# Kernel tuning notes

Hardware: AMD Instinct MI355X
Metric: run time of the kernel (lower is better)

The kernel has to match this reference:

```python
import jax, jax.numpy as jnp
import numpy as np

_J6 = jnp.array([[0, 0, 0, 0, 0, 1], [0, 0, 0, 0, -1, 0], [0, 0, 0, 1, 0, 0],
                 [0, 0, 1, 0, 0, 0], [0, -1, 0, 0, 0, 0], [1, 0, 0, 0, 0, 0]], dtype=jnp.float32)
_PAIRS4 = [(0, 1), (0, 2), (0, 3), (1, 2), (1, 3), (2, 3)]


def exterior(p1, p2):
    # p1, p2: (B,T,H,4) -> (B,T,H,6) normalized Pluecker line coordinates
    parts = [p1[..., i] * p2[..., j] - p1[..., j] * p2[..., i] for i, j in _PAIRS4]
    L = jnp.stack(parts, axis=-1)
    n = jnp.sqrt(jnp.sum(L * L, axis=-1, keepdims=True))
    return L / jnp.maximum(n, 1e-12)


def setup_inputs() -> dict:
    D, H = 1024, 16
    B, T = 2, 2048
    key = jax.random.key(0)
    ks = jax.random.split(key, 16)
    s = 0.02
    return {
        'x': jax.random.normal(ks[0], (B, T, D), dtype=jnp.float32),
        'qkv_w': jax.random.normal(ks[1], (D, 3 * D), dtype=jnp.float32) * s,
        'qkv_b': jnp.zeros((3 * D,), dtype=jnp.float32),
        'w1_write': jax.random.normal(ks[2], (D, 4 * H), dtype=jnp.float32) * s,
        'w2_write': jax.random.normal(ks[3], (D, 4 * H), dtype=jnp.float32) * s,
        'w1_read': jax.random.normal(ks[4], (D, 4 * H), dtype=jnp.float32) * s,
        'w2_read': jax.random.normal(ks[5], (D, 4 * H), dtype=jnp.float32) * s,
        'geo_w': jax.random.normal(ks[6], (D, D), dtype=jnp.float32) * s,
        'geo_b': jnp.zeros((D,), dtype=jnp.float32),
        'gate_w': jax.random.normal(ks[7], (D, H), dtype=jnp.float32) * s,
        'gate_b': jnp.zeros((H,), dtype=jnp.float32),
        'inc_scale': jnp.ones((H,), dtype=jnp.float32),
        'out_w': jax.random.normal(ks[8], (D, D), dtype=jnp.float32) * s,
        'out_b': jnp.zeros((D,), dtype=jnp.float32),
    }


def reference(x, qkv_w, qkv_b, w1_write, w2_write, w1_read, w2_read,
              geo_w, geo_b, gate_w, gate_b, inc_scale, out_w, out_b):
    B, T, D = x.shape
    H = inc_scale.shape[0]
    dh = D // H
    scale = dh ** -0.5

    qkv = (x @ qkv_w + qkv_b).reshape(B, T, 3, H, dh)
    qkv = jnp.transpose(qkv, (2, 0, 3, 1, 4))  # (3,B,H,T,dh)
    q, k, v = qkv[0], qkv[1], qkv[2]

    std_logits = jnp.einsum('bhqd,bhkd->bhqk', q, k) * scale

    x_prev = jnp.concatenate([jnp.zeros((B, 1, D), dtype=x.dtype), x[:, :-1]], axis=1)
    w1 = (x_prev @ w1_write).reshape(B, T, H, 4)
    w2 = (x @ w2_write).reshape(B, T, H, 4)
    write_lines = exterior(w1, w2)  # (B,T,H,6)
    r1 = (x @ w1_read).reshape(B, T, H, 4)
    r2 = (x @ w2_read).reshape(B, T, H, 4)
    read_lines = exterior(r1, r2)  # (B,T,H,6)

    J_write = jnp.einsum('bthi,ij->bthj', write_lines, _J6)  # (B,T,H,6)
    geo_logits = jnp.einsum('bqhi,bkhi->bhqk', read_lines, J_write)
    geo_logits = geo_logits * inc_scale.reshape(1, H, 1, 1)

    mask = jnp.triu(jnp.ones((T, T), dtype=bool), k=1)  # True above diagonal
    neg = jnp.float32(-jnp.inf)

    std_attn = jax.nn.softmax(jnp.where(mask, neg, std_logits), axis=-1)
    std_out = jnp.einsum('bhqk,bhkd->bqhd', std_attn, v).reshape(B, T, D)

    geo_attn = jax.nn.softmax(jnp.where(mask, neg, geo_logits), axis=-1)
    geo_v = (x @ geo_w + geo_b).reshape(B, T, H, dh)
    geo_out = jnp.einsum('bhqk,bkhd->bqhd', geo_attn, geo_v).reshape(B, T, D)

    gate = jax.nn.sigmoid(x @ gate_w + gate_b)  # (B,T,H)
    gate = jnp.mean(gate, axis=-1, keepdims=True)  # (B,T,1)

    combined = (1.0 - gate) * std_out + gate * geo_out
    return combined @ out_w + out_b
```

## Files before the change

### kernel.cpp

```cpp
#include <hip/hip_runtime.h>
#include <hip/hip_bf16.h>

#define Bc 2
#define Tc 2048
#define Dc 1024
#define Hc 16
#define Mc (Bc*Tc)
#define QB 64
#define KB 32
#define NALL 4480

typedef __attribute__((ext_vector_type(8))) short bf16x8;
typedef __attribute__((ext_vector_type(4))) short bf16x4;
typedef __attribute__((ext_vector_type(4))) float fx4;

__device__ __forceinline__ short f2bf(float f) {
  __hip_bfloat16 h = __float2bfloat16(f);
  return *reinterpret_cast<short*>(&h);
}
__device__ __forceinline__ float bf2f(short s) {
  unsigned int u = ((unsigned int)(unsigned short)s) << 16;
  float f;
  __builtin_memcpy(&f, &u, 4);
  return f;
}
__device__ __forceinline__ short p2bf(float f) {
  unsigned int u;
  __builtin_memcpy(&u, &f, 4);
  return (short)((u + 0x8000u) >> 16);
}
__device__ __forceinline__ int pk2bf(float a, float b) {
  unsigned int ua, ub;
  __builtin_memcpy(&ua, &a, 4);
  __builtin_memcpy(&ub, &b, 4);
  return (int)(((ua + 0x8000u) >> 16) | (((ub + 0x8000u) >> 16) << 16));
}

#define MFMA(a, b, c) __builtin_amdgcn_mfma_f32_16x16x32_bf16((a), (b), (c), 0, 0, 0)

#define GLD16(G, L) __builtin_amdgcn_global_load_lds( \
    (const __attribute__((address_space(1))) unsigned int*)(G), \
    (__attribute__((address_space(3))) unsigned int*)(L), 16, 0, 0)

__global__ __launch_bounds__(256) void prep_k(
    const float* __restrict__ x,
    const float* __restrict__ qkv_w, const float* __restrict__ geow,
    const float* __restrict__ w1w, const float* __restrict__ w2w,
    const float* __restrict__ w1r, const float* __restrict__ w2r,
    const float* __restrict__ gatew, const float* __restrict__ outw,
    const float* __restrict__ qkv_b, const float* __restrict__ geob,
    const float* __restrict__ gateb,
    short* __restrict__ xb, short* __restrict__ wtall,
    short* __restrict__ wtout, float* __restrict__ ball)
{
  __shared__ float tile[32][33];
  const int blk = blockIdx.x;

  if (blk < 4096) {
    const int i = blk * 256 + threadIdx.x;
    const float4 v = ((const float4*)x)[i];
    bf16x4 o;
    o[0] = f2bf(v.x); o[1] = f2bf(v.y); o[2] = f2bf(v.z); o[3] = f2bf(v.w);
    ((bf16x4*)xb)[i] = o;
    return;
  }
  if (blk < 8576) {
    const int b2 = blk - 4096;
    const int n0 = (b2 % 140) * 32, k0 = (b2 / 140) * 32;
    const int tx = threadIdx.x & 31, ty = threadIdx.x >> 5;
    const int n = n0 + tx;
    const float* src = nullptr; int ln = 0, sN = 0;
    if (n < 3072)      { src = qkv_w; ln = n;        sN = 3072; }
    else if (n < 4096) { src = geow;  ln = n - 3072; sN = 1024; }
    else if (n < 4160) { src = w1w;   ln = n - 4096; sN = 64; }
    else if (n < 4224) { src = w2w;   ln = n - 4160; sN = 64; }
    else if (n < 4288) { src = w1r;   ln = n - 4224; sN = 64; }
    else if (n < 4352) { src = w2r;   ln = n - 4288; sN = 64; }
    else if (n < 4368) { src = gatew; ln = n - 4352; sN = 16; }
    #pragma unroll
    for (int i = 0; i < 4; i++)
      tile[ty * 4 + i][tx] = src ? src[(size_t)(k0 + ty * 4 + i) * sN + ln] : 0.f;
    __syncthreads();
    #pragma unroll
    for (int i = 0; i < 4; i++) {
      const int nn = n0 + ty * 4 + i;
      const float s = (nn < 1024) ? 0.125f : 1.f;
      wtall[(size_t)nn * 1024 + k0 + tx] = f2bf(tile[tx][ty * 4 + i] * s);
    }
    return;
  }
  if (blk < 9600) {
    const int b3 = blk - 8576;
    const int n0 = (b3 & 31) * 32, k0 = (b3 >> 5) * 32;
    const int tx = threadIdx.x & 31, ty = threadIdx.x >> 5;
    #pragma unroll
    for (int i = 0; i < 4; i++)
      tile[ty * 4 + i][tx] = outw[(size_t)(k0 + ty * 4 + i) * 1024 + n0 + tx];
    __syncthreads();
    #pragma unroll
    for (int i = 0; i < 4; i++)
      wtout[(size_t)(n0 + ty * 4 + i) * 1024 + k0 + tx] = f2bf(tile[tx][ty * 4 + i]);
    return;
  }
  {
    const int n = (blk - 9600) * 256 + threadIdx.x;
    if (n >= NALL) return;
    float v = 0.f;
    if (n < 1024)      v = qkv_b[n] * 0.125f;
    else if (n < 3072) v = qkv_b[n];
    else if (n < 4096) v = geob[n - 3072];
    else if (n >= 4352 && n < 4368) v = gateb[n - 4352];
    ball[n] = v;
  }
}

template<bool BF16_OUT>
__global__ __launch_bounds__(256) void gemm_mfma_k(
    const short* __restrict__ A, const short* __restrict__ Bt,
    const float* __restrict__ bias, void* __restrict__ Cv,
    int M, int N, int K)
{
  __shared__ short As[128][32];
  __shared__ short Bs[128][32];
  const int orig = blockIdx.x + blockIdx.y * gridDim.x;
  const int q8 = (gridDim.x * gridDim.y) >> 3;
  const int idx = (orig & 7) * q8 + (orig >> 3);
  const int m0 = (idx / gridDim.x) * 128, n0 = (idx % gridDim.x) * 128;
  const int tid = threadIdx.x;
  const int wave = tid >> 6, lane = tid & 63;
  const int l15 = lane & 15, lg = lane >> 4;
  const int wm = wave >> 1, wn = wave & 1;
  const int srow = lane >> 2;
  const int schk = (lane & 3) * 8;

  const size_t aBase = (size_t)(m0 + wave * 16 + srow) * K + schk;
  const size_t bBase = (size_t)(n0 + wave * 16 + srow) * K + schk;

  fx4 acc[4][4] = {};

  for (int k0 = 0; k0 < K; k0 += 32) {
    __syncthreads();
    GLD16(&A[aBase + k0],              &As[wave * 16][0]);
    GLD16(&A[aBase + (size_t)64 * K + k0], &As[64 + wave * 16][0]);
    GLD16(&Bt[bBase + k0],             &Bs[wave * 16][0]);
    GLD16(&Bt[bBase + (size_t)64 * K + k0], &Bs[64 + wave * 16][0]);
    __syncthreads();
    bf16x8 af[4], bf[4];
    #pragma unroll
    for (int i = 0; i < 4; i++) {
      af[i] = *(const bf16x8*)&As[wm * 64 + i * 16 + l15][8 * lg];
      bf[i] = *(const bf16x8*)&Bs[wn * 64 + i * 16 + l15][8 * lg];
    }
    #pragma unroll
    for (int i = 0; i < 4; i++)
      #pragma unroll
      for (int j = 0; j < 4; j++)
        acc[i][j] = MFMA(af[i], bf[j], acc[i][j]);
  }

  #pragma unroll
  for (int i = 0; i < 4; i++)
    #pragma unroll
    for (int j = 0; j < 4; j++) {
      const int n = n0 + wn * 64 + j * 16 + l15;
      const float bv = bias ? bias[n] : 0.f;
      #pragma unroll
      for (int rg = 0; rg < 4; rg++) {
        const int m = m0 + wm * 64 + i * 16 + lg * 4 + rg;
        const float v = acc[i][j][rg] + bv;
        if constexpr (BF16_OUT)
          ((short*)Cv)[(size_t)m * N + n] = f2bf(v);
        else
          ((float*)Cv)[(size_t)m * N + n] = v;
      }
    }
}

template<bool BF16_OUT>
__global__ __launch_bounds__(256) void gemm_mfma64_k(
    const short* __restrict__ A, const short* __restrict__ Bt,
    const float* __restrict__ bias, void* __restrict__ Cv,
    int M, int N, int K)
{
  __shared__ short As[64][32];
  __shared__ short Bs[128][32];
  const int orig = blockIdx.x + blockIdx.y * gridDim.x;
  const int q8 = (gridDim.x * gridDim.y) >> 3;
  const int idx = (orig & 7) * q8 + (orig >> 3);
  const int m0 = (idx / gridDim.x) * 64, n0 = (idx % gridDim.x) * 128;
  const int tid = threadIdx.x;
  const int wave = tid >> 6, lane = tid & 63;
  const int l15 = lane & 15, lg = lane >> 4;
  const int srow = lane >> 2;
  const int schk = (lane & 3) * 8;

  const size_t aBase = (size_t)(m0 + wave * 16 + srow) * K + schk;
  const size_t bBase = (size_t)(n0 + wave * 16 + srow) * K + schk;

  fx4 acc[4][2] = {};

  for (int k0 = 0; k0 < K; k0 += 32) {
    __syncthreads();
    GLD16(&A[aBase + k0],                   &As[wave * 16][0]);
    GLD16(&Bt[bBase + k0],                  &Bs[wave * 16][0]);
    GLD16(&Bt[bBase + (size_t)64 * K + k0], &Bs[64 + wave * 16][0]);
    __syncthreads();
    bf16x8 af[4], bf[2];
    #pragma unroll
    for (int i = 0; i < 4; i++)
      af[i] = *(const bf16x8*)&As[i * 16 + l15][8 * lg];
    #pragma unroll
    for (int j = 0; j < 2; j++)
      bf[j] = *(const bf16x8*)&Bs[wave * 32 + j * 16 + l15][8 * lg];
    #pragma unroll
    for (int i = 0; i < 4; i++)
      #pragma unroll
      for (int j = 0; j < 2; j++)
        acc[i][j] = MFMA(af[i], bf[j], acc[i][j]);
  }

  #pragma unroll
  for (int i = 0; i < 4; i++)
    #pragma unroll
    for (int j = 0; j < 2; j++) {
      const int n = n0 + wave * 32 + j * 16 + l15;
      const float bv = bias ? bias[n] : 0.f;
      #pragma unroll
      for (int rg = 0; rg < 4; rg++) {
        const int m = m0 + i * 16 + lg * 4 + rg;
        const float v = acc[i][j][rg] + bv;
        if constexpr (BF16_OUT)
          ((short*)Cv)[(size_t)m * N + n] = f2bf(v);
        else
          ((float*)Cv)[(size_t)m * N + n] = v;
      }
    }
}

__device__ __forceinline__ void exterior6(const float a[4], const float c[4], float L[6]) {
  L[0] = a[0]*c[1] - a[1]*c[0];
  L[1] = a[0]*c[2] - a[2]*c[0];
  L[2] = a[0]*c[3] - a[3]*c[0];
  L[3] = a[1]*c[2] - a[2]*c[1];
  L[4] = a[1]*c[3] - a[3]*c[1];
  L[5] = a[2]*c[3] - a[3]*c[2];
}

__device__ __forceinline__ void load4bf(const short* p, float o[4]) {
  const bf16x4 v = *(const bf16x4*)p;
  o[0] = bf2f(v[0]); o[1] = bf2f(v[1]); o[2] = bf2f(v[2]); o[3] = bf2f(v[3]);
}

__global__ void lines_k(const short* __restrict__ allb,
                        const float* __restrict__ incs,
                        short* __restrict__ JWb, short* __restrict__ RLb,
                        float* __restrict__ gatev)
{
  const int idx = blockIdx.x * 256 + threadIdx.x;
  if (idx >= Bc * Tc * Hc) return;
  const int h = idx & 15;
  const int t = (idx >> 4) & (Tc - 1);
  const int b = idx >> 15;
  const size_t row = (size_t)b * Tc + t;
  const size_t lrow = ((size_t)(b * Hc + h) * Tc + t) * 8;

  float a[4] = {0.f, 0.f, 0.f, 0.f};
  float c[4];
  load4bf(&allb[row * NALL + 4160 + h * 4], c);
  if (t > 0) load4bf(&allb[(row - 1) * NALL + 4096 + h * 4], a);

  float L[6];
  exterior6(a, c, L);
  float n = sqrtf(L[0]*L[0] + L[1]*L[1] + L[2]*L[2] + L[3]*L[3] + L[4]*L[4] + L[5]*L[5]);
  float inv = 1.f / fmaxf(n, 1e-12f);
  const float s = incs[h];
  bf16x8 jw;
  jw[0] = f2bf( L[5] * inv * s);
  jw[1] = f2bf(-L[4] * inv * s);
  jw[2] = f2bf( L[3] * inv * s);
  jw[3] = f2bf( L[2] * inv * s);
  jw[4] = f2bf(-L[1] * inv * s);
  jw[5] = f2bf( L[0] * inv * s);
  jw[6] = 0; jw[7] = 0;
  *(bf16x8*)&JWb[lrow] = jw;

  load4bf(&allb[row * NALL + 4224 + h * 4], a);
  load4bf(&allb[row * NALL + 4288 + h * 4], c);
  exterior6(a, c, L);
  n = sqrtf(L[0]*L[0] + L[1]*L[1] + L[2]*L[2] + L[3]*L[3] + L[4]*L[4] + L[5]*L[5]);
  inv = 1.f / fmaxf(n, 1e-12f);
  bf16x8 rl;
  #pragma unroll
  for (int i = 0; i < 6; i++) rl[i] = f2bf(L[i] * inv);
  rl[6] = 0; rl[7] = 0;
  *(bf16x8*)&RLb[lrow] = rl;

  if (h == 0) {
    float ssum = 0.f;
    #pragma unroll
    for (int hh = 0; hh < 16; hh++) {
      const float v = bf2f(allb[row * NALL + 4352 + hh]);
      ssum += 1.f / (1.f + __expf(-v));
    }
    gatev[row] = ssum * (1.f / 16.f);
  }
}

#define LOADK(K0, a0, a1, b0, b1) { \
  const size_t rb0 = (size_t)(b * Tc + (K0) + l15) * NALL + 1024 + h * 64; \
  const size_t rb1 = rb0 + (size_t)16 * NALL; \
  a0 = *(const bf16x8*)&allb[rb0 + lg * 8]; \
  a1 = *(const bf16x8*)&allb[rb0 + 32 + lg * 8]; \
  b0 = *(const bf16x8*)&allb[rb1 + lg * 8]; \
  b1 = *(const bf16x8*)&allb[rb1 + 32 + lg * 8]; }

#define LOADJW(K0, j0, j1) { \
  j0 = z8; j1 = z8; \
  if (lg == 0) { \
    j0 = *(const bf16x8*)&JWb[(size_t)(bh * Tc + (K0) + l15) * 8]; \
    j1 = *(const bf16x8*)&JWb[(size_t)(bh * Tc + (K0) + 16 + l15) * 8]; \
  } }

#define LOADVG(K0, vr, gr) { \
  vr = *(const bf16x8*)&allb[(size_t)(b * Tc + (K0) + kk) * NALL + 2048 + h * 64 + dg]; \
  gr = *(const bf16x8*)&allb[(size_t)(b * Tc + (K0) + kk) * NALL + 3072 + h * 64 + dg]; }

#define STAGEVG(CUR, vr, gr) { \
  _Pragma("unroll") for (int j = 0; j < 8; j++) { \
    const int d = dg + j; \
    Vt[CUR][d][pcol] = vr[j]; Gt[CUR][d][pcol] = gr[j]; \
  } }

#define COMPUTE(K0, CUR, ka0, ka1, kb0, kb1, jw0, jw1) \
  if ((K0) <= qhi) { \
    fx4 z = {0.f, 0.f, 0.f, 0.f}; \
    fx4 sS0, sS1, sG0, sG1; \
    __builtin_amdgcn_s_setprio(1); \
    sS0 = MFMA(qf0, ka0, z); sS0 = MFMA(qf1, ka1, sS0); \
    sS1 = MFMA(qf0, kb0, z); sS1 = MFMA(qf1, kb1, sS1); \
    sG0 = MFMA(rlf, jw0, z); sG1 = MFMA(rlf, jw1, z); \
    __builtin_amdgcn_s_setprio(0); \
    if ((K0) + KB - 1 > q0 + wave * 16) { \
      const int kg0 = (K0) + l15, kg1 = (K0) + 16 + l15; \
      _Pragma("unroll") for (int r = 0; r < 4; r++) { \
        const int qg = q0 + wave * 16 + lg * 4 + r; \
        if (kg0 > qg) { sS0[r] = -1e30f; sG0[r] = -1e30f; } \
        if (kg1 > qg) { sS1[r] = -1e30f; sG1[r] = -1e30f; } \
      } } \
    _Pragma("unroll") for (int r = 0; r < 4; r++) { \
      const int ql = lg * 4 + r; \
      const float p0 = __expf(sS0[r]); const float p1 = __expf(sS1[r]); \
      lpS[r] += p0 + p1; \
      *(int*)&Ps[wave][ql][2 * l15] = pk2bf(p0, p1); \
      const float g0 = __expf(sG0[r]); const float g1 = __expf(sG1[r]); \
      lpG[r] += g0 + g1; \
      *(int*)&Pg[wave][ql][2 * l15] = pk2bf(g0, g1); \
    } \
    const bf16x8 pa  = *(const bf16x8*)&Ps[wave][l15][8 * lg]; \
    const bf16x8 pga = *(const bf16x8*)&Pg[wave][l15][8 * lg]; \
    __builtin_amdgcn_s_setprio(1); \
    _Pragma("unroll") for (int dt = 0; dt < 4; dt++) { \
      const int dV = dt * 16 + l15; \
      const int swz = 8 * (lg ^ ((dV >> 3) & 3)); \
      accS[dt] = MFMA(pa,  *(const bf16x8*)&Vt[CUR][dV][swz], accS[dt]); \
      accG[dt] = MFMA(pga, *(const bf16x8*)&Gt[CUR][dV][swz], accG[dt]); \
    } \
    __builtin_amdgcn_s_setprio(0); \
  }

__global__ __launch_bounds__(256) void attn3_k(
    const short* __restrict__ allb,
    const short* __restrict__ RLb,
    const short* __restrict__ JWb,
    const float* __restrict__ gate,
    short* __restrict__ combb)
{
  const int orig = blockIdx.x;
  const int xcd  = orig & 7;
  const int idx  = orig >> 3;
  const int pairIdx = idx & 15;
  const int bh   = xcd + 8 * (idx >> 4);
  const int b = bh >> 4, h = bh & 15;
  const int tid = threadIdx.x;
  const int wave = tid >> 6;
  const int lane = tid & 63;
  const int l15 = lane & 15;
  const int lg  = lane >> 4;
  const int kk  = tid >> 3;
  const int dg  = (tid & 7) * 8;
  const int ps_ = 2 * (kk & 15) + (kk >> 4);
  const int pcol = (((ps_ >> 3) ^ ((dg >> 3) & 3)) << 3) | (ps_ & 7);

  __shared__ short Vt[2][64][40];
  __shared__ short Gt[2][64][40];
  __shared__ short Ps[4][16][40];
  __shared__ short Pg[4][16][40];

  const bf16x8 z8 = {0, 0, 0, 0, 0, 0, 0, 0};

  for (int half = 0; half < 2; half++) {
    const int qt = half ? (31 - pairIdx) : pairIdx;
    const int q0 = qt * QB;
    const int nkt = 2 * qt + 2;
    const int qrow = wave * 16 + l15;
    const int qhi = q0 + wave * 16 + 15;

    const size_t qrb = (size_t)(b * Tc + q0 + qrow) * NALL + h * 64;
    const bf16x8 qf0 = *(const bf16x8*)&allb[qrb + lg * 8];
    const bf16x8 qf1 = *(const bf16x8*)&allb[qrb + 32 + lg * 8];
    bf16x8 rlf = z8;
    if (lg == 0) rlf = *(const bf16x8*)&RLb[(size_t)(bh * Tc + q0 + qrow) * 8];

    fx4 accS[4] = {}, accG[4] = {};
    float lpS[4] = {0.f, 0.f, 0.f, 0.f};
    float lpG[4] = {0.f, 0.f, 0.f, 0.f};

    bf16x8 kA0a, kA1a, kB0a, kB1a, jw0a, jw1a, vrA, grA;
    bf16x8 kA0b, kA1b, kB0b, kB1b, jw0b, jw1b, vrB, grB;
    LOADK(0, kA0a, kA1a, kB0a, kB1a);
    LOADJW(0, jw0a, jw1a);
    LOADVG(0, vrA, grA);

    __syncthreads();

    for (int kt = 0; kt < nkt; kt += 2) {
      const int k0a = kt * KB, k0b = k0a + KB;
      STAGEVG(0, vrA, grA);
      LOADK(k0b, kA0b, kA1b, kB0b, kB1b);
      LOADJW(k0b, jw0b, jw1b);
      LOADVG(k0b, vrB, grB);
      __syncthreads();
      COMPUTE(k0a, 0, kA0a, kA1a, kB0a, kB1a, jw0a, jw1a);
      STAGEVG(1, vrB, grB);
      if (kt + 2 < nkt) {
        LOADK(k0b + KB, kA0a, kA1a, kB0a, kB1a);
        LOADJW(k0b + KB, jw0a, jw1a);
        LOADVG(k0b + KB, vrA, grA);
      }
      __syncthreads();
      COMPUTE(k0b, 1, kA0b, kA1b, kB0b, kB1b, jw0b, jw1b);
    }

    #pragma unroll
    for (int r = 0; r < 4; r++) {
      float ls = lpS[r];
      ls += __shfl_xor(ls, 1); ls += __shfl_xor(ls, 2);
      ls += __shfl_xor(ls, 4); ls += __shfl_xor(ls, 8);
      float lgeo = lpG[r];
      lgeo += __shfl_xor(lgeo, 1); lgeo += __shfl_xor(lgeo, 2);
      lgeo += __shfl_xor(lgeo, 4); lgeo += __shfl_xor(lgeo, 8);
      const int qg = q0 + wave * 16 + lg * 4 + r;
      const float gt = gate[(size_t)b * Tc + qg];
      const float invS = (1.f - gt) / ls;
      const float invG = gt / lgeo;
      #pragma unroll
      for (int dt = 0; dt < 4; dt++) {
        const float o = accS[dt][r] * invS + accG[dt][r] * invG;
        combb[(size_t)(b * Tc + qg) * 1024 + h * 64 + dt * 16 + l15] = f2bf(o);
      }
    }
  }
}

extern "C" void kernel_launch(void* const* d_in, const int* in_sizes, int n_in,
                              void* d_out, int out_size, void* d_ws, size_t ws_size,
                              hipStream_t stream) {
  (void)in_sizes; (void)n_in; (void)out_size; (void)ws_size;
  const float* x     = (const float*)d_in[0];
  const float* qkv_w = (const float*)d_in[1];
  const float* qkv_b = (const float*)d_in[2];
  const float* w1w   = (const float*)d_in[3];
  const float* w2w   = (const float*)d_in[4];
  const float* w1r   = (const float*)d_in[5];
  const float* w2r   = (const float*)d_in[6];
  const float* geow  = (const float*)d_in[7];
  const float* geob  = (const float*)d_in[8];
  const float* gatew = (const float*)d_in[9];
  const float* gateb = (const float*)d_in[10];
  const float* incs  = (const float*)d_in[11];
  const float* outw  = (const float*)d_in[12];
  const float* outb  = (const float*)d_in[13];
  float* out = (float*)d_out;

  char* p = (char*)d_ws;
  short* xb    = (short*)p;  p += (size_t)4096 * 1024 * 2;
  short* wtall = (short*)p;  p += (size_t)NALL * 1024 * 2;
  short* allb  = (short*)p;  p += (size_t)4096 * NALL * 2;
  short* combb = (short*)p;  p += (size_t)4096 * 1024 * 2;
  short* wtout = (short*)p;  p += (size_t)1024 * 1024 * 2;
  short* JWb   = (short*)p;  p += (size_t)32 * 2048 * 8 * 2;
  short* RLb   = (short*)p;  p += (size_t)32 * 2048 * 8 * 2;
  float* ball  = (float*)p;  p += (size_t)NALL * 4;
  float* gatev = (float*)p;  p += (size_t)4096 * 4;

  const dim3 blk(256);

  prep_k<<<dim3(9618), blk, 0, stream>>>(x, qkv_w, geow, w1w, w2w, w1r, w2r,
                                         gatew, outw, qkv_b, geob, gateb,
                                         xb, wtall, wtout, ball);

  gemm_mfma_k<true><<<dim3(NALL / 128, 32), blk, 0, stream>>>(xb, wtall, ball, allb, 4096, NALL, 1024);

  lines_k<<<dim3((Bc * Tc * Hc + 255) / 256), blk, 0, stream>>>(allb, incs, JWb, RLb, gatev);

  attn3_k<<<dim3(512), blk, 0, stream>>>(allb, RLb, JWb, gatev, combb);

  gemm_mfma64_k<false><<<dim3(8, 64), blk, 0, stream>>>(combb, wtout, outb, (void*)out, 4096, 1024, 1024);
}
```

Measured before the change: 191.0 us.

## Double attention key block size to 64 and restructure pipeline

Raises the key tile from 32 to 64 rows per iteration in the fused standard/geometric attention kernel, so each step computes four 16-column score groups and twice the PV MFMAs per staged tile. This halves the number of iterations and the __syncthreads barriers per query tile. Shared buffers are widened to 72 columns, and the loop now handles an odd tile count with an early break plus a trailing barrier. In exchange it needs more registers for the prefetched K/V/G fragments, which may lower occupancy, and the diagonal tile does more masked work.

```diff
diff --git a/kernel.cpp b/kernel.cpp
--- a/kernel.cpp
+++ b/kernel.cpp
@@ -7,7 +7,7 @@
 #define Hc 16
 #define Mc (Bc*Tc)
 #define QB 64
-#define KB 32
+#define KB 64
 #define NALL 4480
 
 typedef __attribute__((ext_vector_type(8))) short bf16x8;
@@ -23,11 +23,6 @@
   float f;
   __builtin_memcpy(&f, &u, 4);
   return f;
-}
-__device__ __forceinline__ short p2bf(float f) {
-  unsigned int u;
-  __builtin_memcpy(&u, &f, 4);
-  return (short)((u + 0x8000u) >> 16);
 }
 __device__ __forceinline__ int pk2bf(float a, float b) {
   unsigned int ua, ub;
@@ -306,64 +301,73 @@
   }
 }
 
-#define LOADK(K0, a0, a1, b0, b1) { \
-  const size_t rb0 = (size_t)(b * Tc + (K0) + l15) * NALL + 1024 + h * 64; \
-  const size_t rb1 = rb0 + (size_t)16 * NALL; \
-  a0 = *(const bf16x8*)&allb[rb0 + lg * 8]; \
-  a1 = *(const bf16x8*)&allb[rb0 + 32 + lg * 8]; \
-  b0 = *(const bf16x8*)&allb[rb1 + lg * 8]; \
-  b1 = *(const bf16x8*)&allb[rb1 + 32 + lg * 8]; }
-
-#define LOADJW(K0, j0, j1) { \
-  j0 = z8; j1 = z8; \
-  if (lg == 0) { \
-    j0 = *(const bf16x8*)&JWb[(size_t)(bh * Tc + (K0) + l15) * 8]; \
-    j1 = *(const bf16x8*)&JWb[(size_t)(bh * Tc + (K0) + 16 + l15) * 8]; \
+#define LOADK64(K0, kf, jw) { \
+  _Pragma("unroll") for (int cg = 0; cg < 4; cg++) { \
+    const size_t rb = (size_t)(b * Tc + (K0) + cg * 16 + l15) * NALL + 1024 + h * 64; \
+    kf[cg][0] = *(const bf16x8*)&allb[rb + lg * 8]; \
+    kf[cg][1] = *(const bf16x8*)&allb[rb + 32 + lg * 8]; \
+    jw[cg] = z8; \
+    if (lg == 0) jw[cg] = *(const bf16x8*)&JWb[(size_t)(bh * Tc + (K0) + cg * 16 + l15) * 8]; \
   } }
 
-#define LOADVG(K0, vr, gr) { \
-  vr = *(const bf16x8*)&allb[(size_t)(b * Tc + (K0) + kk) * NALL + 2048 + h * 64 + dg]; \
-  gr = *(const bf16x8*)&allb[(size_t)(b * Tc + (K0) + kk) * NALL + 3072 + h * 64 + dg]; }
-
-#define STAGEVG(CUR, vr, gr) { \
+#define LOADVG64(K0, v0, v1, g0, g1) { \
+  const size_t r0 = (size_t)(b * Tc + (K0) + kk) * NALL + h * 64 + dg; \
+  const size_t r1 = (size_t)(b * Tc + (K0) + kk + 32) * NALL + h * 64 + dg; \
+  v0 = *(const bf16x8*)&allb[r0 + 2048]; \
+  g0 = *(const bf16x8*)&allb[r0 + 3072]; \
+  v1 = *(const bf16x8*)&allb[r1 + 2048]; \
+  g1 = *(const bf16x8*)&allb[r1 + 3072]; }
+
+#define STAGEVG64(CUR, v0, v1, g0, g1) { \
   _Pragma("unroll") for (int j = 0; j < 8; j++) { \
     const int d = dg + j; \
-    Vt[CUR][d][pcol] = vr[j]; Gt[CUR][d][pcol] = gr[j]; \
+    Vt[CUR][d][pcol]      = v0[j]; Gt[CUR][d][pcol]      = g0[j]; \
+    Vt[CUR][d][32 + pcol] = v1[j]; Gt[CUR][d][32 + pcol] = g1[j]; \
   } }
 
-#define COMPUTE(K0, CUR, ka0, ka1, kb0, kb1, jw0, jw1) \
+#define COMPUTE64(K0, CUR, kf, jw) \
   if ((K0) <= qhi) { \
     fx4 z = {0.f, 0.f, 0.f, 0.f}; \
-    fx4 sS0, sS1, sG0, sG1; \
+    fx4 sS[4], sG[4]; \
     __builtin_amdgcn_s_setprio(1); \
-    sS0 = MFMA(qf0, ka0, z); sS0 = MFMA(qf1, ka1, sS0); \
-    sS1 = MFMA(qf0, kb0, z); sS1 = MFMA(qf1, kb1, sS1); \
-    sG0 = MFMA(rlf, jw0, z); sG1 = MFMA(rlf, jw1, z); \
+    _Pragma("unroll") for (int cg = 0; cg < 4; cg++) { \
+      sS[cg] = MFMA(qf0, kf[cg][0], z); \
+      sS[cg] = MFMA(qf1, kf[cg][1], sS[cg]); \
+      sG[cg] = MFMA(rlf, jw[cg], z); \
+    } \
     __builtin_amdgcn_s_setprio(0); \
     if ((K0) + KB - 1 > q0 + wave * 16) { \
-      const int kg0 = (K0) + l15, kg1 = (K0) + 16 + l15; \
-      _Pragma("unroll") for (int r = 0; r < 4; r++) { \
-        const int qg = q0 + wave * 16 + lg * 4 + r; \
-        if (kg0 > qg) { sS0[r] = -1e30f; sG0[r] = -1e30f; } \
-        if (kg1 > qg) { sS1[r] = -1e30f; sG1[r] = -1e30f; } \
-      } } \
+      _Pragma("unroll") for (int cg = 0; cg < 4; cg++) { \
+        const int kg = (K0) + cg * 16 + l15; \
+        _Pragma("unroll") for (int r = 0; r < 4; r++) { \
+          const int qg = q0 + wave * 16 + lg * 4 + r; \
+          if (kg > qg) { sS[cg][r] = -1e30f; sG[cg][r] = -1e30f; } \
+        } } } \
     _Pragma("unroll") for (int r = 0; r < 4; r++) { \
       const int ql = lg * 4 + r; \
-      const float p0 = __expf(sS0[r]); const float p1 = __expf(sS1[r]); \
-      lpS[r] += p0 + p1; \
-      *(int*)&Ps[wave][ql][2 * l15] = pk2bf(p0, p1); \
-      const float g0 = __expf(sG0[r]); const float g1 = __expf(sG1[r]); \
-      lpG[r] += g0 + g1; \
-      *(int*)&Pg[wave][ql][2 * l15] = pk2bf(g0, g1); \
+      const float p0 = __expf(sS[0][r]); const float p1 = __expf(sS[1][r]); \
+      const float p2 = __expf(sS[2][r]); const float p3 = __expf(sS[3][r]); \
+      lpS[r] += (p0 + p1) + (p2 + p3); \
+      *(int*)&Ps[wave][ql][2 * l15]      = pk2bf(p0, p1); \
+      *(int*)&Ps[wave][ql][32 + 2 * l15] = pk2bf(p2, p3); \
+      const float g0 = __expf(sG[0][r]); const float g1 = __expf(sG[1][r]); \
+      const float g2 = __expf(sG[2][r]); const float g3 = __expf(sG[3][r]); \
+      lpG[r] += (g0 + g1) + (g2 + g3); \
+      *(int*)&Pg[wave][ql][2 * l15]      = pk2bf(g0, g1); \
+      *(int*)&Pg[wave][ql][32 + 2 * l15] = pk2bf(g2, g3); \
     } \
-    const bf16x8 pa  = *(const bf16x8*)&Ps[wave][l15][8 * lg]; \
-    const bf16x8 pga = *(const bf16x8*)&Pg[wave][l15][8 * lg]; \
+    const bf16x8 paL  = *(const bf16x8*)&Ps[wave][l15][8 * lg]; \
+    const bf16x8 paH  = *(const bf16x8*)&Ps[wave][l15][32 + 8 * lg]; \
+    const bf16x8 pgaL = *(const bf16x8*)&Pg[wave][l15][8 * lg]; \
+    const bf16x8 pgaH = *(const bf16x8*)&Pg[wave][l15][32 + 8 * lg]; \
     __builtin_amdgcn_s_setprio(1); \
     _Pragma("unroll") for (int dt = 0; dt < 4; dt++) { \
       const int dV = dt * 16 + l15; \
-      const int swz = 8 * (lg ^ ((dV >> 3) & 3)); \
-      accS[dt] = MFMA(pa,  *(const bf16x8*)&Vt[CUR][dV][swz], accS[dt]); \
-      accG[dt] = MFMA(pga, *(const bf16x8*)&Gt[CUR][dV][swz], accG[dt]); \
+      const int sw = 8 * (lg ^ ((dV >> 3) & 3)); \
+      accS[dt] = MFMA(paL, *(const bf16x8*)&Vt[CUR][dV][sw],      accS[dt]); \
+      accS[dt] = MFMA(paH, *(const bf16x8*)&Vt[CUR][dV][32 + sw], accS[dt]); \
+      accG[dt] = MFMA(pgaL, *(const bf16x8*)&Gt[CUR][dV][sw],      accG[dt]); \
+      accG[dt] = MFMA(pgaH, *(const bf16x8*)&Gt[CUR][dV][32 + sw], accG[dt]); \
     } \
     __builtin_amdgcn_s_setprio(0); \
   }
@@ -391,17 +395,17 @@
   const int ps_ = 2 * (kk & 15) + (kk >> 4);
   const int pcol = (((ps_ >> 3) ^ ((dg >> 3) & 3)) << 3) | (ps_ & 7);
 
-  __shared__ short Vt[2][64][40];
-  __shared__ short Gt[2][64][40];
-  __shared__ short Ps[4][16][40];
-  __shared__ short Pg[4][16][40];
+  __shared__ short Vt[2][64][72];
+  __shared__ short Gt[2][64][72];
+  __shared__ short Ps[4][16][72];
+  __shared__ short Pg[4][16][72];
 
   const bf16x8 z8 = {0, 0, 0, 0, 0, 0, 0, 0};
 
   for (int half = 0; half < 2; half++) {
     const int qt = half ? (31 - pairIdx) : pairIdx;
     const int q0 = qt * QB;
-    const int nkt = 2 * qt + 2;
+    const int nkt = qt + 1;
     const int qrow = wave * 16 + l15;
     const int qhi = q0 + wave * 16 + 15;
 
@@ -415,31 +419,32 @@
     float lpS[4] = {0.f, 0.f, 0.f, 0.f};
     float lpG[4] = {0.f, 0.f, 0.f, 0.f};
 
-    bf16x8 kA0a, kA1a, kB0a, kB1a, jw0a, jw1a, vrA, grA;
-    bf16x8 kA0b, kA1b, kB0b, kB1b, jw0b, jw1b, vrB, grB;
-    LOADK(0, kA0a, kA1a, kB0a, kB1a);
-    LOADJW(0, jw0a, jw1a);
-    LOADVG(0, vrA, grA);
+    bf16x8 kfA[4][2], jwA[4], kfB[4][2], jwB[4];
+    bf16x8 vA0, vA1, gA0, gA1, vB0, vB1, gB0, gB1;
+
+    LOADK64(0, kfA, jwA);
+    LOADVG64(0, vA0, vA1, gA0, gA1);
 
     __syncthreads();
 
     for (int kt = 0; kt < nkt; kt += 2) {
-      const int k0a = kt * KB, k0b = k0a + KB;
-      STAGEVG(0, vrA, grA);
-      LOADK(k0b, kA0b, kA1b, kB0b, kB1b);
-      LOADJW(k0b, jw0b, jw1b);
-      LOADVG(k0b, vrB, grB);
-      __syncthreads();
-      COMPUTE(k0a, 0, kA0a, kA1a, kB0a, kB1a, jw0a, jw1a);
-      STAGEVG(1, vrB, grB);
-      if (kt + 2 < nkt) {
-        LOADK(k0b + KB, kA0a, kA1a, kB0a, kB1a);
-        LOADJW(k0b + KB, jw0a, jw1a);
-        LOADVG(k0b + KB, vrA, grA);
+      STAGEVG64(0, vA0, vA1, gA0, gA1);
+      if (kt + 1 < nkt) {
+        LOADK64((kt + 1) * KB, kfB, jwB);
+        LOADVG64((kt + 1) * KB, vB0, vB1, gB0, gB1);
       }
       __syncthreads();
-      COMPUTE(k0b, 1, kA0b, kA1b, kB0b, kB1b, jw0b, jw1b);
-    }
+      COMPUTE64(kt * KB, 0, kfA, jwA);
+      if (kt + 1 >= nkt) break;
+      STAGEVG64(1, vB0, vB1, gB0, gB1);
+      if (kt + 2 < nkt) {
+        LOADK64((kt + 2) * KB, kfA, jwA);
+        LOADVG64((kt + 2) * KB, vA0, vA1, gA0, gA1);
+      }
+      __syncthreads();
+      COMPUTE64((kt + 1) * KB, 1, kfB, jwB);
+    }
+    __syncthreads();
 
     #pragma unroll
     for (int r = 0; r < 4; r++) {
```

Result: slower. 261.8 us (+37.1%).
